# Performance work log

Measured on AMD Instinct MI355X. Metric: run time of the kernel, lower is better.

## Reference

```python
import jax, jax.numpy as jnp
import numpy as np
import math

G, T, D, B = 20000, 1536, 512, 256
TOPK = 32


def setup_inputs() -> dict:
    key = jax.random.key(0)
    k1, k2, k3, k4 = jax.random.split(key, 4)
    tg_dec = jax.random.normal(k1, (G, D), dtype=jnp.float32)
    tf_base = jax.random.normal(k2, (T, D), dtype=jnp.float32)
    tf_expr = jax.random.normal(k3, (B, T), dtype=jnp.float32)
    motif_mask = jax.random.randint(k4, (G, T), 0, 2).astype(jnp.int32)
    scale = jnp.full((1,), 0.1, dtype=jnp.float32)  # nn.Parameter scale
    return {"tg_dec": tg_dec, "tf_base": tf_base, "tf_expr": tf_expr,
            "motif_mask": motif_mask, "scale": scale}


def reference(tg_dec, tf_base, tf_expr, motif_mask, scale):
    # scaled similarity: [G, T]
    sim = jnp.matmul(tg_dec, tf_base.T) / math.sqrt(tf_base.shape[1])
    # masked fill where motif prior is absent
    sim = jnp.where(motif_mask == 0, -jnp.inf, sim)
    attn = jax.nn.softmax(sim, axis=-1)
    attn = jnp.nan_to_num(attn, nan=0.0)
    # top-k selection + scatter mask + renormalize
    _, topk_idx = jax.lax.top_k(attn, TOPK)              # [G, TOPK]
    rows = jnp.arange(attn.shape[0])[:, None]
    mask = jnp.zeros_like(attn).at[rows, topk_idx].set(1.0)
    attn = attn * mask
    attn = attn / (attn.sum(axis=-1, keepdims=True) + 1e-8)
    # weighted combine: [B, G]
    tf_scalar = jnp.matmul(tf_expr, attn.T)
    # dropout is identity in eval mode
    return (scale[0] * tf_scalar, attn)
```

## Files before the change

### kernel.cpp

```cpp
#include <hip/hip_runtime.h>
#include <cstdint>

typedef unsigned short u16;
typedef unsigned int   u32;
typedef unsigned long long u64;

#define G_ROWS 20000
#define G_PAD  20096
#define T_DIM  1536
#define D_DIM  512
#define B_DIM  256
#define TOPK   32
#define SIM_SCALE 0.04419417382415922f
#define SQRT_D    22.62741699796952f
#define BOUND_EPS 2.0e-4f

typedef __bf16 bf16x8 __attribute__((ext_vector_type(8)));
typedef float  f32x4  __attribute__((ext_vector_type(4)));

__device__ __forceinline__ u16 f2bf(float f) {
  u32 u = __float_as_uint(f);
  u += 0x7fffu + ((u >> 16) & 1u);
  return (u16)(u >> 16);
}
__device__ __forceinline__ float bf2f(u16 h) {
  return __uint_as_float(((u32)h) << 16);
}
__device__ __forceinline__ u32 fkey(float v) {
  u32 b = __float_as_uint(v);
  return (b & 0x80000000u) ? ~b : (b | 0x80000000u);
}
__device__ __forceinline__ float funkey(u32 o) {
  u32 b = (o & 0x80000000u) ? (o & 0x7FFFFFFFu) : ~o;
  return __uint_as_float(b);
}

__global__ __launch_bounds__(256) void conv_split(const float* __restrict__ src,
                                                  u16* __restrict__ hi, u16* __restrict__ lo,
                                                  int valid_rows)
{
  size_t i = ((size_t)blockIdx.x * 256 + threadIdx.x) * 4;
  int row = (int)(i >> 9);
  float4 a = make_float4(0.f, 0.f, 0.f, 0.f);
  if (row < valid_rows) a = *(const float4*)(src + i);
  float v[4] = {a.x, a.y, a.z, a.w};
  u16 h[4], l[4];
#pragma unroll
  for (int c = 0; c < 4; ++c) {
    h[c] = f2bf(v[c]);
    l[c] = f2bf(v[c] - bf2f(h[c]));
  }
  *(uint2*)(hi + i) = make_uint2((u32)h[0] | ((u32)h[1] << 16), (u32)h[2] | ((u32)h[3] << 16));
  *(uint2*)(lo + i) = make_uint2((u32)l[0] | ((u32)l[1] << 16), (u32)l[2] | ((u32)l[3] << 16));
}

__global__ __launch_bounds__(256) void transpose_tf(const float* __restrict__ in, float* __restrict__ out)
{
  __shared__ float tile[32][33];
  int x = threadIdx.x, y = threadIdx.y;
  int bt = blockIdx.x * 32;
  int bb = blockIdx.y * 32;
#pragma unroll
  for (int i = 0; i < 32; i += 8) tile[y + i][x] = in[(size_t)(bb + y + i) * T_DIM + bt + x];
  __syncthreads();
#pragma unroll
  for (int i = 0; i < 32; i += 8) out[(size_t)(bt + y + i) * B_DIM + bb + x] = tile[x][y + i];
}

__device__ __forceinline__ void gl16(const u16* g, u16* l) {
  __builtin_amdgcn_global_load_lds((__attribute__((address_space(1))) void*)(void*)g,
                                   (__attribute__((address_space(3))) void*)l, 16, 0, 0);
}

#define BMT 256
#define BNT 128
#define NBX 12
#define NWG 948
#define LDS_HALF 24576

__global__ __launch_bounds__(512, 2) void gemm_split(const u16* __restrict__ Ah, const u16* __restrict__ Al,
                                                     const u16* __restrict__ Bh, const u16* __restrict__ Bl,
                                                     float* __restrict__ Sim)
{
  __shared__ u16 sm[2 * LDS_HALF];

  const int orig = blockIdx.x;
  const int xcd  = orig & 7;
  const int q    = NWG >> 3, r = NWG & 7;
  const int wgid = (xcd < r ? xcd * (q + 1) : r * (q + 1) + (xcd - r) * q) + (orig >> 3);
  const int by   = wgid / NBX;
  const int bx   = wgid - by * NBX;
  const int bm0  = by * BMT;
  const int bn0  = bx * BNT;

  const int tid  = threadIdx.x;
  const int lane = tid & 63;
  const int wv   = tid >> 6;
  const int wm   = wv >> 1;
  const int wn   = wv & 1;

  const size_t aOff = (size_t)(bm0 + (wv << 4) + (lane & 15)) * 512 + ((lane >> 4) << 3);
  const size_t bOff = (size_t)(bn0 + (wv << 4) + (lane & 15)) * 512 + ((lane >> 4) << 3);

  f32x4 zero4 = {0.f, 0.f, 0.f, 0.f};
  f32x4 acc[4][4];
#pragma unroll
  for (int i = 0; i < 4; ++i)
#pragma unroll
    for (int j = 0; j < 4; ++j) acc[i][j] = zero4;

#define STAGE(pb, kt) do {                                         \
    u16* d = sm + (pb) * LDS_HALF + ((wv) << 9);                   \
    const int k0s = (kt) << 5;                                     \
    gl16(Ah + aOff + k0s,         d);                              \
    gl16(Ah + aOff + k0s + 65536, d + 4096);                       \
    gl16(Al + aOff + k0s,         d + 8192);                       \
    gl16(Al + aOff + k0s + 65536, d + 12288);                      \
    gl16(Bh + bOff + k0s,         d + 16384);                      \
    gl16(Bl + bOff + k0s,         d + 20480);                      \
  } while (0)

  STAGE(0, 0);

#pragma unroll
  for (int kt = 0; kt < 16; ++kt) {
    const int pb = kt & 1;
    if (kt < 15) {
      STAGE(pb ^ 1, kt + 1);
      asm volatile("s_waitcnt vmcnt(6)" ::: "memory");
    } else {
      asm volatile("s_waitcnt vmcnt(0)" ::: "memory");
    }
    __builtin_amdgcn_s_barrier();
    __builtin_amdgcn_sched_barrier(0);

    const u16* rb = sm + pb * LDS_HALF;
    const int la8 = lane << 3;
    bf16x8 aH[4], aL[4], bH[4], bL[4];
#pragma unroll
    for (int i = 0; i < 4; ++i) {
      const int sa = ((wm << 2) + i) << 9;
      const int sb = ((wn << 2) + i) << 9;
      aH[i] = *(const bf16x8*)(rb + sa + la8);
      aL[i] = *(const bf16x8*)(rb + 8192 + sa + la8);
      bH[i] = *(const bf16x8*)(rb + 16384 + sb + la8);
      bL[i] = *(const bf16x8*)(rb + 20480 + sb + la8);
    }
    __builtin_amdgcn_s_setprio(1);
#pragma unroll
    for (int mi = 0; mi < 4; ++mi)
#pragma unroll
      for (int ni = 0; ni < 4; ++ni) {
        acc[mi][ni] = __builtin_amdgcn_mfma_f32_16x16x32_bf16(aH[mi], bH[ni], acc[mi][ni], 0, 0, 0);
        acc[mi][ni] = __builtin_amdgcn_mfma_f32_16x16x32_bf16(aH[mi], bL[ni], acc[mi][ni], 0, 0, 0);
        acc[mi][ni] = __builtin_amdgcn_mfma_f32_16x16x32_bf16(aL[mi], bH[ni], acc[mi][ni], 0, 0, 0);
      }
    __builtin_amdgcn_s_setprio(0);
    __builtin_amdgcn_sched_barrier(0);
    __builtin_amdgcn_s_barrier();
  }
#undef STAGE

  const int erow0 = bm0 + (wm << 6) + ((lane >> 4) << 2);
  const int ecol0 = bn0 + (wn << 6) + (lane & 15);
#pragma unroll
  for (int mi = 0; mi < 4; ++mi)
#pragma unroll
    for (int rr = 0; rr < 4; ++rr) {
      int row = erow0 + mi * 16 + rr;
      if (row < G_ROWS) {
#pragma unroll
        for (int ni = 0; ni < 4; ++ni)
          Sim[(size_t)row * T_DIM + ecol0 + ni * 16] = acc[mi][ni][rr] * SIM_SCALE;
      }
    }
}

__device__ __forceinline__ int count_ge(const float* v, float tau) {
  int c = 0;
#pragma unroll
  for (int j = 0; j < 24; ++j) c += (int)__popcll(__ballot(v[j] >= tau));
  return c;
}
__device__ __forceinline__ u64 bitonic64_desc(u64 key, int lane) {
#pragma unroll
  for (int k = 2; k <= 64; k <<= 1) {
#pragma unroll
    for (int j = k >> 1; j > 0; j >>= 1) {
      u64 p = __shfl_xor(key, j, 64);
      bool lower = (lane & j) == 0;
      bool asc   = (lane & k) != 0;
      u64 mn = (key < p) ? key : p;
      u64 mx = (key < p) ? p : key;
      key = (lower == asc) ? mn : mx;
    }
  }
  return key;
}

__global__ __launch_bounds__(256) void topk_kernel(float* __restrict__ Sim, const int* __restrict__ mask,
                                                   const float* __restrict__ tg_dec,
                                                   const float* __restrict__ tf_base,
                                                   int* __restrict__ tIdx, float* __restrict__ tW)
{
  __shared__ u32 cval[4][64];
  __shared__ int cidxs[4][64];
  const int lane = threadIdx.x & 63;
  const int wv   = threadIdx.x >> 6;
  const int g    = blockIdx.x * 4 + wv;
  float* row = Sim + (size_t)g * T_DIM;
  const int* mrow = mask + (size_t)g * T_DIM;

  float v[24];
#pragma unroll
  for (int j = 0; j < 6; ++j) {
    float4 q = *(const float4*)(row + j * 256 + lane * 4);
    int4  mq = *(const int4*)(mrow + j * 256 + lane * 4);
    v[j * 4 + 0] = mq.x ? q.x : -INFINITY;
    v[j * 4 + 1] = mq.y ? q.y : -INFINITY;
    v[j * 4 + 2] = mq.z ? q.z : -INFINITY;
    v[j * 4 + 3] = mq.w ? q.w : -INFINITY;
  }

  const float TH0 = 1.25f, TH1 = 1.40f, TH2 = 1.55f, TH3 = 1.70f, TH4 = 1.85f, TH5 = 2.00f;
  int n0 = 0, n1 = 0, n2 = 0, n3 = 0, n4 = 0, n5 = 0, nv = 0;
#pragma unroll
  for (int j = 0; j < 24; ++j) {
    float x = v[j];
    n0 += (x >= TH0); n1 += (x >= TH1); n2 += (x >= TH2);
    n3 += (x >= TH3); n4 += (x >= TH4); n5 += (x >= TH5);
    nv += (x != -INFINITY);
  }
  u64 p0 = (u64)(u32)n0 | ((u64)(u32)n1 << 16) | ((u64)(u32)n2 << 32) | ((u64)(u32)n3 << 48);
  u64 p1 = (u64)(u32)n4 | ((u64)(u32)n5 << 16) | ((u64)(u32)nv << 32);
#pragma unroll
  for (int off = 32; off > 0; off >>= 1) {
    p0 += __shfl_xor(p0, off, 64);
    p1 += __shfl_xor(p1, off, 64);
  }
  int c[6];
  c[0] = (int)(p0 & 0xFFFF); c[1] = (int)((p0 >> 16) & 0xFFFF);
  c[2] = (int)((p0 >> 32) & 0xFFFF); c[3] = (int)((p0 >> 48) & 0xFFFF);
  c[4] = (int)(p1 & 0xFFFF); c[5] = (int)((p1 >> 16) & 0xFFFF);
  const int cvalid = (int)((p1 >> 32) & 0xFFFF);

  float tau; int cnt;
  if (cvalid <= 64) { tau = -3.0e38f; cnt = cvalid; }
  else {
    int is = -1;
#pragma unroll
    for (int i = 0; i < 6; ++i) if (c[i] >= 33) is = i;
    const float THv[7] = {TH0, TH1, TH2, TH3, TH4, TH5, 8.0f};
    if (is >= 0 && c[is] <= 64) { tau = THv[is]; cnt = c[is]; }
    else {
      float lo, hi;
      if (is < 0) { lo = -4.0f; hi = TH0; }
      else        { lo = THv[is]; hi = THv[is + 1]; }
      tau = lo; cnt = 1000;
      for (int it = 0; it < 16; ++it) {
        float mid = 0.5f * (lo + hi);
        int cm = count_ge(v, mid);
        if (cm > 64)      lo = mid;
        else if (cm < 33) hi = mid;
        else { tau = mid; cnt = cm; break; }
      }
      if (cnt == 1000) tau = lo;
    }
  }

  int base = 0;
#pragma unroll
  for (int j = 0; j < 24; ++j) {
    bool pred = (v[j] >= tau);
    u64 bmc = __ballot(pred);
    int pos = base + (int)__popcll(bmc & ((1ull << lane) - 1ull));
    int idx = (j >> 2) * 256 + lane * 4 + (j & 3);
    if (pred && pos < 64) { cval[wv][pos] = fkey(v[j]); cidxs[wv][pos] = idx; }
    base += (int)__popcll(bmc);
  }
  const int cnt_eff = (base < 64) ? base : 64;

  u64 key = 0;
  if (lane < cnt_eff)
    key = ((u64)cval[wv][lane] << 32) | (u64)(u32)(~(u32)cidxs[wv][lane]);

  key = bitonic64_desc(key, lane);
  int   myidx = (int)(~(u32)key);
  float myv   = (key != 0) ? funkey((u32)(key >> 32)) : -INFINITY;

  float v31 = __shfl(myv, 31, 64);
  float v32 = __shfl(myv, 32, 64);
  if (cnt_eff > TOPK && (v31 - v32) < 2.0f * BOUND_EPS) {
    bool flag = (lane < cnt_eff) &&
                (myv >= v32 - 2.0f * BOUND_EPS) && (myv <= v31 + 2.0f * BOUND_EPS);
    if (flag) {
      const float* arow_g = tg_dec + (size_t)g * D_DIM;
      const float* brow   = tf_base + (size_t)myidx * D_DIM;
      float s1 = 0.f, s2 = 0.f;
#pragma unroll 8
      for (int k = 0; k < 384; k += 4) {
        float4 av = *(const float4*)(arow_g + k);
        float4 bv = *(const float4*)(brow + k);
        s1 = fmaf(av.x, bv.x, s1); s1 = fmaf(av.y, bv.y, s1);
        s1 = fmaf(av.z, bv.z, s1); s1 = fmaf(av.w, bv.w, s1);
      }
#pragma unroll 8
      for (int k = 384; k < 512; k += 4) {
        float4 av = *(const float4*)(arow_g + k);
        float4 bv = *(const float4*)(brow + k);
        s2 = fmaf(av.x, bv.x, s2); s2 = fmaf(av.y, bv.y, s2);
        s2 = fmaf(av.z, bv.z, s2); s2 = fmaf(av.w, bv.w, s2);
      }
      myv = (s1 + s2) / SQRT_D;
      key = ((u64)fkey(myv) << 32) | (u64)(u32)(~(u32)myidx);
    }
    key = bitonic64_desc(key, lane);
    myidx = (int)(~(u32)key);
    myv   = (key != 0) ? funkey((u32)(key >> 32)) : -INFINITY;
  }

  const bool selme = (lane < TOPK) && (lane < cnt_eff);
  float mx = __shfl(myv, 0, 64);
  float e = selme ? __expf(myv - mx) : 0.f;
  float E = e;
#pragma unroll
  for (int off = 32; off > 0; off >>= 1) E += __shfl_xor(E, off, 64);
  float rden = (E > 0.f) ? (1.f / E) : 0.f;
  float w = e * rden;

  const float4 z4 = make_float4(0.f, 0.f, 0.f, 0.f);
#pragma unroll
  for (int j = 0; j < 6; ++j) *(float4*)(row + j * 256 + lane * 4) = z4;
  asm volatile("s_waitcnt vmcnt(0)" ::: "memory");
  if (selme) row[myidx] = w;

  if (cnt_eff < TOPK && lane >= cnt_eff && lane < TOPK) {
    tIdx[(size_t)g * TOPK + lane] = 0; tW[(size_t)g * TOPK + lane] = 0.f;
  }
  if (selme) {
    tIdx[(size_t)g * TOPK + lane] = myidx;
    tW[(size_t)g * TOPK + lane]   = w;
  }
}

__global__ __launch_bounds__(256) void combine_kernel(const float* __restrict__ tfT, const int* __restrict__ tIdx,
                                                      const float* __restrict__ tW, const float* __restrict__ scalep,
                                                      float* __restrict__ out0)
{
  __shared__ int   sIdx[16 * 32];
  __shared__ float sW[16 * 32];
  const int tid = threadIdx.x;
  const int g0 = blockIdx.x * 16;
  for (int i = tid; i < 512; i += 256) {
    sIdx[i] = tIdx[(size_t)g0 * 32 + i];
    sW[i]   = tW[(size_t)g0 * 32 + i];
  }
  __syncthreads();
  const float scale = scalep[0];
  float acc[16];
#pragma unroll
  for (int gi = 0; gi < 16; ++gi) acc[gi] = 0.f;
#pragma unroll 4
  for (int gi = 0; gi < 16; ++gi) {
    float a = 0.f;
#pragma unroll
    for (int k = 0; k < 32; ++k) {
      float w = sW[gi * 32 + k];
      int t   = sIdx[gi * 32 + k];
      a += w * tfT[(size_t)t * B_DIM + tid];
    }
    acc[gi] = a;
  }
  float* dst = out0 + (size_t)tid * G_ROWS + g0;
#pragma unroll
  for (int q = 0; q < 4; ++q) {
    float4 o = make_float4(scale * acc[4*q], scale * acc[4*q+1], scale * acc[4*q+2], scale * acc[4*q+3]);
    *(float4*)(dst + 4 * q) = o;
  }
}

extern "C" void kernel_launch(void* const* d_in, const int* in_sizes, int n_in,
                              void* d_out, int out_size, void* d_ws, size_t ws_size,
                              hipStream_t stream)
{
  const float* tg_dec     = (const float*)d_in[0];
  const float* tf_base    = (const float*)d_in[1];
  const float* tf_expr    = (const float*)d_in[2];
  const int*   motif_mask = (const int*)d_in[3];
  const float* scale      = (const float*)d_in[4];

  float* out0 = (float*)d_out;
  float* attn = out0 + (size_t)B_DIM * G_ROWS;

  char* ws = (char*)d_ws;
  u16*   Ah    = (u16*)(ws);
  u16*   Al    = (u16*)(ws + 20578304);
  u16*   Bh    = (u16*)(ws + 41156608);
  u16*   Bl    = (u16*)(ws + 42729472);
  float* tfT   = (float*)(ws + 44302336);
  int*   tIdx  = (int*)(ws + 45875200);
  float* tW    = (float*)(ws + 48435200);

  conv_split<<<10048, 256, 0, stream>>>(tg_dec, Ah, Al, G_ROWS);
  conv_split<<<768,   256, 0, stream>>>(tf_base, Bh, Bl, T_DIM);
  transpose_tf<<<dim3(48, 8), dim3(32, 8), 0, stream>>>(tf_expr, tfT);
  gemm_split<<<NWG, 512, 0, stream>>>(Ah, Al, Bh, Bl, attn);
  topk_kernel<<<5000, 256, 0, stream>>>(attn, motif_mask, tg_dec, tf_base, tIdx, tW);
  combine_kernel<<<1250, 256, 0, stream>>>(tfT, tIdx, tW, scale, out0);
}
```

Before: 456.8 us.

## Split GEMM k-step into three phased MFMA passes with staged hi/lo prefetch

Restructures the split-bf16 GEMM main loop so each k-step runs three separate MFMA passes (hi*hi, lo*hi, hi*lo). LDS reads for each pass are interleaved with the MFMA work, and the hi and lo global-to-LDS prefetches for the next tile are issued in separate phases. The aim is to overlap LDS reads and global loads with matrix-core work and lower register pressure from holding all fragments at once. In exchange it adds several more workgroup barriers per iteration, which could cost more synchronization stalls. It also changes the accumulation order of the three products.

```diff
diff --git a/kernel.cpp b/kernel.cpp
--- a/kernel.cpp
+++ b/kernel.cpp
@@ -72,8 +72,6 @@
                                    (__attribute__((address_space(3))) void*)l, 16, 0, 0);
 }
 
-#define BMT 256
-#define BNT 128
 #define NBX 12
 #define NWG 948
 #define LDS_HALF 24576
@@ -90,8 +88,8 @@
   const int wgid = (xcd < r ? xcd * (q + 1) : r * (q + 1) + (xcd - r) * q) + (orig >> 3);
   const int by   = wgid / NBX;
   const int bx   = wgid - by * NBX;
-  const int bm0  = by * BMT;
-  const int bn0  = bx * BNT;
+  const int bm0  = by * 256;
+  const int bn0  = bx * 128;
 
   const int tid  = threadIdx.x;
   const int lane = tid & 63;
@@ -109,57 +107,92 @@
 #pragma unroll
     for (int j = 0; j < 4; ++j) acc[i][j] = zero4;
 
-#define STAGE(pb, kt) do {                                         \
+#define STAGE_HI(pb, kt) do {                                      \
     u16* d = sm + (pb) * LDS_HALF + ((wv) << 9);                   \
     const int k0s = (kt) << 5;                                     \
     gl16(Ah + aOff + k0s,         d);                              \
     gl16(Ah + aOff + k0s + 65536, d + 4096);                       \
+    gl16(Bh + bOff + k0s,         d + 16384);                      \
+  } while (0)
+#define STAGE_LO(pb, kt) do {                                      \
+    u16* d = sm + (pb) * LDS_HALF + ((wv) << 9);                   \
+    const int k0s = (kt) << 5;                                     \
     gl16(Al + aOff + k0s,         d + 8192);                       \
     gl16(Al + aOff + k0s + 65536, d + 12288);                      \
-    gl16(Bh + bOff + k0s,         d + 16384);                      \
     gl16(Bl + bOff + k0s,         d + 20480);                      \
   } while (0)
 
-  STAGE(0, 0);
+  STAGE_HI(0, 0);
+  STAGE_LO(0, 0);
+  asm volatile("s_waitcnt vmcnt(3)" ::: "memory");
+  __builtin_amdgcn_s_barrier();
+
+  const int la8 = lane << 3;
 
 #pragma unroll
   for (int kt = 0; kt < 16; ++kt) {
     const int pb = kt & 1;
+    const u16* rb = sm + pb * LDS_HALF;
+    bf16x8 aH[4], bH[4], aL[4], bL[4];
+
+#pragma unroll
+    for (int i = 0; i < 4; ++i) {
+      aH[i] = *(const bf16x8*)(rb +         ((((wm << 2) + i) << 9)) + la8);
+      bH[i] = *(const bf16x8*)(rb + 16384 + ((((wn << 2) + i) << 9)) + la8);
+    }
     if (kt < 15) {
-      STAGE(pb ^ 1, kt + 1);
-      asm volatile("s_waitcnt vmcnt(6)" ::: "memory");
+      STAGE_HI(pb ^ 1, kt + 1);
+      asm volatile("s_waitcnt vmcnt(3)" ::: "memory");
     } else {
       asm volatile("s_waitcnt vmcnt(0)" ::: "memory");
     }
     __builtin_amdgcn_s_barrier();
+    asm volatile("s_waitcnt lgkmcnt(0)" ::: "memory");
     __builtin_amdgcn_sched_barrier(0);
-
-    const u16* rb = sm + pb * LDS_HALF;
-    const int la8 = lane << 3;
-    bf16x8 aH[4], aL[4], bH[4], bL[4];
-#pragma unroll
-    for (int i = 0; i < 4; ++i) {
-      const int sa = ((wm << 2) + i) << 9;
-      const int sb = ((wn << 2) + i) << 9;
-      aH[i] = *(const bf16x8*)(rb + sa + la8);
-      aL[i] = *(const bf16x8*)(rb + 8192 + sa + la8);
-      bH[i] = *(const bf16x8*)(rb + 16384 + sb + la8);
-      bL[i] = *(const bf16x8*)(rb + 20480 + sb + la8);
-    }
     __builtin_amdgcn_s_setprio(1);
 #pragma unroll
     for (int mi = 0; mi < 4; ++mi)
 #pragma unroll
-      for (int ni = 0; ni < 4; ++ni) {
+      for (int ni = 0; ni < 4; ++ni)
         acc[mi][ni] = __builtin_amdgcn_mfma_f32_16x16x32_bf16(aH[mi], bH[ni], acc[mi][ni], 0, 0, 0);
+    __builtin_amdgcn_s_setprio(0);
+    __builtin_amdgcn_s_barrier();
+
+#pragma unroll
+    for (int i = 0; i < 4; ++i)
+      aL[i] = *(const bf16x8*)(rb + 8192 + ((((wm << 2) + i) << 9)) + la8);
+    if (kt < 15) STAGE_LO(pb ^ 1, kt + 1);
+    __builtin_amdgcn_s_barrier();
+    asm volatile("s_waitcnt lgkmcnt(0)" ::: "memory");
+    __builtin_amdgcn_sched_barrier(0);
+    __builtin_amdgcn_s_setprio(1);
+#pragma unroll
+    for (int mi = 0; mi < 4; ++mi)
+#pragma unroll
+      for (int ni = 0; ni < 4; ++ni)
+        acc[mi][ni] = __builtin_amdgcn_mfma_f32_16x16x32_bf16(aL[mi], bH[ni], acc[mi][ni], 0, 0, 0);
+    __builtin_amdgcn_s_setprio(0);
+    __builtin_amdgcn_s_barrier();
+
+#pragma unroll
+    for (int i = 0; i < 4; ++i)
+      bL[i] = *(const bf16x8*)(rb + 20480 + ((((wn << 2) + i) << 9)) + la8);
+    if (kt < 15)
+      asm volatile("s_waitcnt vmcnt(3)" ::: "memory");
+    __builtin_amdgcn_s_barrier();
+    asm volatile("s_waitcnt lgkmcnt(0)" ::: "memory");
+    __builtin_amdgcn_sched_barrier(0);
+    __builtin_amdgcn_s_setprio(1);
+#pragma unroll
+    for (int mi = 0; mi < 4; ++mi)
+#pragma unroll
+      for (int ni = 0; ni < 4; ++ni)
         acc[mi][ni] = __builtin_amdgcn_mfma_f32_16x16x32_bf16(aH[mi], bL[ni], acc[mi][ni], 0, 0, 0);
-        acc[mi][ni] = __builtin_amdgcn_mfma_f32_16x16x32_bf16(aL[mi], bH[ni], acc[mi][ni], 0, 0, 0);
-      }
     __builtin_amdgcn_s_setprio(0);
-    __builtin_amdgcn_sched_barrier(0);
-    __builtin_amdgcn_s_barrier();
-  }
-#undef STAGE
+    __builtin_amdgcn_s_barrier();
+  }
+#undef STAGE_HI
+#undef STAGE_LO
 
   const int erow0 = bm0 + (wm << 6) + ((lane >> 4) << 2);
   const int ecol0 = bn0 + (wn << 6) + (lane & 15);
```

Measured after the change: 452.5 us. About the same (-1.0%).

## Enlarge GEMM tile to 256x256 with quarter-staged pipeline and fuse prep kernels

Applied to the files above, without the earlier changes.

The three preprocessing launches (A split, B split, tf_expr transpose) are merged into one kernel to cut launch overhead. The split-bf16 GEMM tile grows from 256x128 to 256x256, with eight waves in a 2x4 layout each holding 8x4 accumulators. This raises data reuse per LDS load and halves the workgroup count. The K loop is split into four MFMA quarters, with A and B staged separately and global-to-LDS loads interleaved between them. The cost is higher register pressure under the 2-per-CU launch bound, 128KB of LDS per block, and fewer workgroups (474) to spread across CUs.

```diff
diff --git a/kernel.cpp b/kernel.cpp
--- a/kernel.cpp
+++ b/kernel.cpp
@@ -35,36 +35,44 @@
   return __uint_as_float(b);
 }
 
-__global__ __launch_bounds__(256) void conv_split(const float* __restrict__ src,
-                                                  u16* __restrict__ hi, u16* __restrict__ lo,
-                                                  int valid_rows)
-{
-  size_t i = ((size_t)blockIdx.x * 256 + threadIdx.x) * 4;
-  int row = (int)(i >> 9);
-  float4 a = make_float4(0.f, 0.f, 0.f, 0.f);
-  if (row < valid_rows) a = *(const float4*)(src + i);
-  float v[4] = {a.x, a.y, a.z, a.w};
-  u16 h[4], l[4];
-#pragma unroll
-  for (int c = 0; c < 4; ++c) {
-    h[c] = f2bf(v[c]);
-    l[c] = f2bf(v[c] - bf2f(h[c]));
-  }
-  *(uint2*)(hi + i) = make_uint2((u32)h[0] | ((u32)h[1] << 16), (u32)h[2] | ((u32)h[3] << 16));
-  *(uint2*)(lo + i) = make_uint2((u32)l[0] | ((u32)l[1] << 16), (u32)l[2] | ((u32)l[3] << 16));
-}
-
-__global__ __launch_bounds__(256) void transpose_tf(const float* __restrict__ in, float* __restrict__ out)
+__global__ __launch_bounds__(256) void prep(const float* __restrict__ tg_dec,
+                                            const float* __restrict__ tf_base,
+                                            const float* __restrict__ tf_expr,
+                                            u16* __restrict__ Ah, u16* __restrict__ Al,
+                                            u16* __restrict__ Bh, u16* __restrict__ Bl,
+                                            float* __restrict__ tfT)
 {
   __shared__ float tile[32][33];
-  int x = threadIdx.x, y = threadIdx.y;
-  int bt = blockIdx.x * 32;
-  int bb = blockIdx.y * 32;
-#pragma unroll
-  for (int i = 0; i < 32; i += 8) tile[y + i][x] = in[(size_t)(bb + y + i) * T_DIM + bt + x];
-  __syncthreads();
-#pragma unroll
-  for (int i = 0; i < 32; i += 8) out[(size_t)(bt + y + i) * B_DIM + bb + x] = tile[x][y + i];
+  const int b = blockIdx.x;
+  const int tid = threadIdx.x;
+  if (b < 10816) {
+    const float* src; u16 *hi, *lo; int valid_rows; int bb;
+    if (b < 10048) { src = tg_dec; hi = Ah; lo = Al; valid_rows = G_ROWS; bb = b; }
+    else           { src = tf_base; hi = Bh; lo = Bl; valid_rows = T_DIM; bb = b - 10048; }
+    size_t i = ((size_t)bb * 256 + tid) * 4;
+    int row = (int)(i >> 9);
+    float4 a = make_float4(0.f, 0.f, 0.f, 0.f);
+    if (row < valid_rows) a = *(const float4*)(src + i);
+    float v[4] = {a.x, a.y, a.z, a.w};
+    u16 h[4], l[4];
+#pragma unroll
+    for (int c = 0; c < 4; ++c) {
+      h[c] = f2bf(v[c]);
+      l[c] = f2bf(v[c] - bf2f(h[c]));
+    }
+    *(uint2*)(hi + i) = make_uint2((u32)h[0] | ((u32)h[1] << 16), (u32)h[2] | ((u32)h[3] << 16));
+    *(uint2*)(lo + i) = make_uint2((u32)l[0] | ((u32)l[1] << 16), (u32)l[2] | ((u32)l[3] << 16));
+  } else {
+    const int t = b - 10816;
+    const int x = tid & 31, y = tid >> 5;
+    const int bt = (t % 48) * 32;
+    const int bb = (t / 48) * 32;
+#pragma unroll
+    for (int i = 0; i < 32; i += 8) tile[y + i][x] = tf_expr[(size_t)(bb + y + i) * T_DIM + bt + x];
+    __syncthreads();
+#pragma unroll
+    for (int i = 0; i < 32; i += 8) tfT[(size_t)(bt + y + i) * B_DIM + bb + x] = tile[x][y + i];
+  }
 }
 
 __device__ __forceinline__ void gl16(const u16* g, u16* l) {
@@ -72,17 +80,14 @@
                                    (__attribute__((address_space(3))) void*)l, 16, 0, 0);
 }
 
-#define BMT 256
-#define BNT 128
-#define NBX 12
-#define NWG 948
-#define LDS_HALF 24576
+#define NBX 6
+#define NWG 474
 
 __global__ __launch_bounds__(512, 2) void gemm_split(const u16* __restrict__ Ah, const u16* __restrict__ Al,
                                                      const u16* __restrict__ Bh, const u16* __restrict__ Bl,
                                                      float* __restrict__ Sim)
 {
-  __shared__ u16 sm[2 * LDS_HALF];
+  __shared__ u16 sm[65536];
 
   const int orig = blockIdx.x;
   const int xcd  = orig & 7;
@@ -90,81 +95,126 @@
   const int wgid = (xcd < r ? xcd * (q + 1) : r * (q + 1) + (xcd - r) * q) + (orig >> 3);
   const int by   = wgid / NBX;
   const int bx   = wgid - by * NBX;
-  const int bm0  = by * BMT;
-  const int bn0  = bx * BNT;
+  const int bm0  = by * 256;
+  const int bn0  = bx * 256;
 
   const int tid  = threadIdx.x;
   const int lane = tid & 63;
   const int wv   = tid >> 6;
-  const int wm   = wv >> 1;
-  const int wn   = wv & 1;
-
-  const size_t aOff = (size_t)(bm0 + (wv << 4) + (lane & 15)) * 512 + ((lane >> 4) << 3);
-  const size_t bOff = (size_t)(bn0 + (wv << 4) + (lane & 15)) * 512 + ((lane >> 4) << 3);
-
-  f32x4 zero4 = {0.f, 0.f, 0.f, 0.f};
-  f32x4 acc[4][4];
-#pragma unroll
-  for (int i = 0; i < 4; ++i)
-#pragma unroll
-    for (int j = 0; j < 4; ++j) acc[i][j] = zero4;
-
-#define STAGE(pb, kt) do {                                         \
-    u16* d = sm + (pb) * LDS_HALF + ((wv) << 9);                   \
-    const int k0s = (kt) << 5;                                     \
-    gl16(Ah + aOff + k0s,         d);                              \
-    gl16(Ah + aOff + k0s + 65536, d + 4096);                       \
-    gl16(Al + aOff + k0s,         d + 8192);                       \
-    gl16(Al + aOff + k0s + 65536, d + 12288);                      \
-    gl16(Bh + bOff + k0s,         d + 16384);                      \
-    gl16(Bl + bOff + k0s,         d + 20480);                      \
+  const int wm   = wv >> 2;
+  const int wn   = wv & 3;
+  const int la8  = lane << 3;
+
+  const int sub  = wv << 1;
+  const int srow = lane & 15;
+  const int skc  = (lane >> 4) << 3;
+  const u16* gA0 = Ah + (size_t)(bm0 + (sub + 0) * 16 + srow) * 512 + skc;
+  const u16* gA1 = Ah + (size_t)(bm0 + (sub + 1) * 16 + srow) * 512 + skc;
+  const u16* gAl0 = Al + (size_t)(bm0 + (sub + 0) * 16 + srow) * 512 + skc;
+  const u16* gAl1 = Al + (size_t)(bm0 + (sub + 1) * 16 + srow) * 512 + skc;
+  const u16* gB0 = Bh + (size_t)(bn0 + (sub + 0) * 16 + srow) * 512 + skc;
+  const u16* gB1 = Bh + (size_t)(bn0 + (sub + 1) * 16 + srow) * 512 + skc;
+  const u16* gBl0 = Bl + (size_t)(bn0 + (sub + 0) * 16 + srow) * 512 + skc;
+  const u16* gBl1 = Bl + (size_t)(bn0 + (sub + 1) * 16 + srow) * 512 + skc;
+
+#define STAGE_A(p, ktn) do {                                   \
+    const size_t ko = (size_t)(ktn) << 5;                      \
+    u16* d = sm + (p) * 16384 + sub * 512;                     \
+    gl16(gA0 + ko,  d);                                        \
+    gl16(gA1 + ko,  d + 512);                                  \
+    gl16(gAl0 + ko, d + 8192);                                 \
+    gl16(gAl1 + ko, d + 8192 + 512);                           \
   } while (0)
-
-  STAGE(0, 0);
-
-#pragma unroll
+#define STAGE_B(p, ktn) do {                                   \
+    const size_t ko = (size_t)(ktn) << 5;                      \
+    u16* d = sm + 32768 + (p) * 16384 + sub * 512;             \
+    gl16(gB0 + ko,  d);                                        \
+    gl16(gB1 + ko,  d + 512);                                  \
+    gl16(gBl0 + ko, d + 8192);                                 \
+    gl16(gBl1 + ko, d + 8192 + 512);                           \
+  } while (0)
+
+  f32x4 acc[8][4];
+#pragma unroll
+  for (int i = 0; i < 8; ++i)
+#pragma unroll
+    for (int j = 0; j < 4; ++j) acc[i][j] = (f32x4){0.f, 0.f, 0.f, 0.f};
+
+  bf16x8 aH[4], aL[4], bH[4], bL[4];
+
+#define READ_A(rbA, half) do {                                                     \
+    _Pragma("unroll")                                                              \
+    for (int i = 0; i < 4; ++i) {                                                  \
+      aH[i] = *(const bf16x8*)((rbA) + (wm * 8 + (half) * 4 + i) * 512 + la8);     \
+      aL[i] = *(const bf16x8*)((rbA) + 8192 + (wm * 8 + (half) * 4 + i) * 512 + la8); \
+    }                                                                              \
+  } while (0)
+#define READ_B(rbB, half) do {                                                     \
+    _Pragma("unroll")                                                              \
+    for (int i = 0; i < 2; ++i) {                                                  \
+      bH[(half) * 2 + i] = *(const bf16x8*)((rbB) + (wn * 4 + (half) * 2 + i) * 512 + la8); \
+      bL[(half) * 2 + i] = *(const bf16x8*)((rbB) + 8192 + (wn * 4 + (half) * 2 + i) * 512 + la8); \
+    }                                                                              \
+  } while (0)
+#define MFMA_Q(qm, qn) do {                                                        \
+    __builtin_amdgcn_s_setprio(1);                                                 \
+    _Pragma("unroll")                                                              \
+    for (int m2 = 0; m2 < 4; ++m2)                                                 \
+      _Pragma("unroll")                                                            \
+      for (int n2 = 0; n2 < 2; ++n2) {                                             \
+        const int mi = (qm) * 4 + m2, ni = (qn) * 2 + n2;                          \
+        acc[mi][ni] = __builtin_amdgcn_mfma_f32_16x16x32_bf16(aH[m2], bH[ni], acc[mi][ni], 0, 0, 0); \
+        acc[mi][ni] = __builtin_amdgcn_mfma_f32_16x16x32_bf16(aH[m2], bL[ni], acc[mi][ni], 0, 0, 0); \
+        acc[mi][ni] = __builtin_amdgcn_mfma_f32_16x16x32_bf16(aL[m2], bH[ni], acc[mi][ni], 0, 0, 0); \
+      }                                                                            \
+    __builtin_amdgcn_s_setprio(0);                                                 \
+  } while (0)
+#define LGKM0 do { asm volatile("s_waitcnt lgkmcnt(0)" ::: "memory"); __builtin_amdgcn_sched_barrier(0); } while (0)
+#define BAR   do { __builtin_amdgcn_sched_barrier(0); __builtin_amdgcn_s_barrier(); } while (0)
+
+  STAGE_A(0, 0);
+  STAGE_B(0, 0);
+  STAGE_A(1, 1);
+
+#pragma unroll 2
   for (int kt = 0; kt < 16; ++kt) {
-    const int pb = kt & 1;
-    if (kt < 15) {
-      STAGE(pb ^ 1, kt + 1);
-      asm volatile("s_waitcnt vmcnt(6)" ::: "memory");
-    } else {
-      asm volatile("s_waitcnt vmcnt(0)" ::: "memory");
-    }
-    __builtin_amdgcn_s_barrier();
-    __builtin_amdgcn_sched_barrier(0);
-
-    const u16* rb = sm + pb * LDS_HALF;
-    const int la8 = lane << 3;
-    bf16x8 aH[4], aL[4], bH[4], bL[4];
-#pragma unroll
-    for (int i = 0; i < 4; ++i) {
-      const int sa = ((wm << 2) + i) << 9;
-      const int sb = ((wn << 2) + i) << 9;
-      aH[i] = *(const bf16x8*)(rb + sa + la8);
-      aL[i] = *(const bf16x8*)(rb + 8192 + sa + la8);
-      bH[i] = *(const bf16x8*)(rb + 16384 + sb + la8);
-      bL[i] = *(const bf16x8*)(rb + 20480 + sb + la8);
-    }
-    __builtin_amdgcn_s_setprio(1);
-#pragma unroll
-    for (int mi = 0; mi < 4; ++mi)
-#pragma unroll
-      for (int ni = 0; ni < 4; ++ni) {
-        acc[mi][ni] = __builtin_amdgcn_mfma_f32_16x16x32_bf16(aH[mi], bH[ni], acc[mi][ni], 0, 0, 0);
-        acc[mi][ni] = __builtin_amdgcn_mfma_f32_16x16x32_bf16(aH[mi], bL[ni], acc[mi][ni], 0, 0, 0);
-        acc[mi][ni] = __builtin_amdgcn_mfma_f32_16x16x32_bf16(aL[mi], bH[ni], acc[mi][ni], 0, 0, 0);
-      }
-    __builtin_amdgcn_s_setprio(0);
-    __builtin_amdgcn_sched_barrier(0);
-    __builtin_amdgcn_s_barrier();
-  }
-#undef STAGE
-
-  const int erow0 = bm0 + (wm << 6) + ((lane >> 4) << 2);
+    const u16* rbA = sm + (kt & 1) * 16384;
+    const u16* rbB = sm + 32768 + (kt & 1) * 16384;
+
+    asm volatile("s_waitcnt vmcnt(4)" ::: "memory");
+    BAR;
+    READ_A(rbA, 0);
+    READ_B(rbB, 0);
+    LGKM0;
+    MFMA_Q(0, 0);
+    BAR;
+
+    if (kt < 15) STAGE_B((kt + 1) & 1, kt + 1);
+    READ_B(rbB, 1);
+    LGKM0;
+    MFMA_Q(0, 1);
+    BAR;
+
+    READ_A(rbA, 1);
+    LGKM0;
+    MFMA_Q(1, 0);
+    BAR;
+
+    if (kt < 14) STAGE_A(kt & 1, kt + 2);
+    MFMA_Q(1, 1);
+  }
+#undef STAGE_A
+#undef STAGE_B
+#undef READ_A
+#undef READ_B
+#undef MFMA_Q
+#undef LGKM0
+#undef BAR
+
+  const int erow0 = bm0 + (wm << 7) + ((lane >> 4) << 2);
   const int ecol0 = bn0 + (wn << 6) + (lane & 15);
 #pragma unroll
-  for (int mi = 0; mi < 4; ++mi)
+  for (int mi = 0; mi < 8; ++mi)
 #pragma unroll
     for (int rr = 0; rr < 4; ++rr) {
       int row = erow0 + mi * 16 + rr;
@@ -401,9 +451,7 @@
   int*   tIdx  = (int*)(ws + 45875200);
   float* tW    = (float*)(ws + 48435200);
 
-  conv_split<<<10048, 256, 0, stream>>>(tg_dec, Ah, Al, G_ROWS);
-  conv_split<<<768,   256, 0, stream>>>(tf_base, Bh, Bl, T_DIM);
-  transpose_tf<<<dim3(48, 8), dim3(32, 8), 0, stream>>>(tf_expr, tfT);
+  prep<<<11200, 256, 0, stream>>>(tg_dec, tf_base, tf_expr, Ah, Al, Bh, Bl, tfT);
   gemm_split<<<NWG, 512, 0, stream>>>(Ah, Al, Bh, Bl, attn);
   topk_kernel<<<5000, 256, 0, stream>>>(attn, motif_mask, tg_dec, tf_base, tIdx, tW);
   combine_kernel<<<1250, 256, 0, stream>>>(tfT, tIdx, tW, scale, out0);
```

New measurement: 425.0 us. -7.0%, faster.
